# Kernel optimization log

Measured on AMD Instinct MI355X. Metric: run time of the kernel, lower is better.

Reference implementation:

```python
import jax, jax.numpy as jnp
import numpy as np

B, L, D = 4, 2048, 1024
DI = D            # d_inner = expand * d_model, expand=1
N = 8             # d_state
K = 4             # d_conv
R = 64            # dt_rank = ceil(d_model/16)
EPS = 1e-5


def setup_inputs() -> dict:
    key = jax.random.key(0)
    ks = jax.random.split(key, 10)
    hidden_states = jax.random.normal(ks[0], (B, L, D), dtype=jnp.float32)
    norm_w = jnp.ones((D,), dtype=jnp.float32)
    in_proj_w = jax.random.normal(ks[1], (2 * DI, D), dtype=jnp.float32) * 0.02
    conv_w = jax.random.normal(ks[2], (DI, 1, K), dtype=jnp.float32) * 0.2
    conv_b = jnp.zeros((DI,), dtype=jnp.float32)
    x_proj_w = jax.random.normal(ks[3], (R + 2 * N, DI), dtype=jnp.float32) * 0.02
    dt_proj_w = jax.random.normal(ks[4], (DI, R), dtype=jnp.float32) * 0.1
    # bias init so softplus(bias) lands in a sane dt range (~e^-4 .. e^-1)
    dt_proj_b = jax.random.uniform(ks[5], (DI,), minval=-4.0, maxval=-1.0, dtype=jnp.float32)
    # S4D-real style init: A = -[1..N] per channel
    A_log = jnp.log(jnp.broadcast_to(jnp.arange(1, N + 1, dtype=jnp.float32), (DI, N)))
    D_skip = jnp.ones((DI,), dtype=jnp.float32)
    out_proj_w = jax.random.normal(ks[6], (D, DI), dtype=jnp.float32) * 0.02
    return {
        "hidden_states": hidden_states, "norm_w": norm_w,
        "in_proj_w": in_proj_w, "conv_w": conv_w, "conv_b": conv_b,
        "x_proj_w": x_proj_w, "dt_proj_w": dt_proj_w, "dt_proj_b": dt_proj_b,
        "A_log": A_log, "D_skip": D_skip, "out_proj_w": out_proj_w,
    }


def _rmsnorm(x, w):
    return x * jax.lax.rsqrt(jnp.mean(x * x, axis=-1, keepdims=True) + EPS) * w


def _mamba_block(hidden_states, norm_w, in_proj_w, conv_w, conv_b,
                 x_proj_w, dt_proj_w, dt_proj_b, A_log, D_skip, out_proj_w):
    x = _rmsnorm(hidden_states, norm_w)                      # [B,L,D]
    xz = jnp.einsum('bld,ed->ble', x, in_proj_w)             # [B,L,2*DI]
    x, z = jnp.split(xz, 2, axis=-1)                         # [B,L,DI] each
    # causal depthwise conv1d (torch pads d_conv-1 both sides then slices :L => left pad only)
    xc = jnp.transpose(x, (0, 2, 1))                         # [B,DI,L]
    k = conv_w.shape[-1]
    xc = jax.lax.conv_general_dilated(
        xc, conv_w, window_strides=(1,), padding=[(k - 1, 0)],
        dimension_numbers=('NCH', 'OIH', 'NCH'), feature_group_count=DI)
    x = jax.nn.silu(jnp.transpose(xc, (0, 2, 1)) + conv_b)   # [B,L,DI]
    # input-dependent dt, B, C
    dbl = jnp.einsum('bld,ed->ble', x, x_proj_w)             # [B,L,R+2N]
    dt, Bm, Cm = jnp.split(dbl, [R, R + N], axis=-1)
    dt = jax.nn.softplus(jnp.einsum('blr,dr->bld', dt, dt_proj_w) + dt_proj_b)  # [B,L,DI]
    A = -jnp.exp(A_log)                                      # [DI,N]
    dA = jnp.exp(dt[..., None] * A)                          # [B,L,DI,N]
    dBx = dt[..., None] * Bm[:, :, None, :] * x[..., None]   # [B,L,DI,N]

    def step(h, inp):
        a_t, bx_t, c_t = inp                                 # [B,DI,N],[B,DI,N],[B,N]
        h = a_t * h + bx_t
        y = jnp.einsum('bdn,bn->bd', h, c_t)
        return h, y

    h0 = jnp.zeros((hidden_states.shape[0], DI, N), dtype=x.dtype)
    _, ys = jax.lax.scan(step, h0, (jnp.transpose(dA, (1, 0, 2, 3)),
                                    jnp.transpose(dBx, (1, 0, 2, 3)),
                                    jnp.transpose(Cm, (1, 0, 2))))
    y = jnp.transpose(ys, (1, 0, 2)) + D_skip * x            # [B,L,DI]
    y = y * jax.nn.silu(z)
    out = jnp.einsum('bld,ed->ble', y, out_proj_w)           # [B,L,D]
    return out  # use_res=False


def reference(hidden_states, norm_w, in_proj_w, conv_w, conv_b,
              x_proj_w, dt_proj_w, dt_proj_b, A_log, D_skip, out_proj_w):
    return _mamba_block(hidden_states, norm_w, in_proj_w, conv_w, conv_b,
                        x_proj_w, dt_proj_w, dt_proj_b, A_log, D_skip, out_proj_w)
```

## Files before the change

### kernel.cpp

```cpp
#include <hip/hip_runtime.h>
#include <stdint.h>
#include <stddef.h>


typedef unsigned short u16;
typedef unsigned int u32;
typedef _Float16 f16;
typedef __attribute__((ext_vector_type(8))) _Float16 half8;
typedef __attribute__((ext_vector_type(4))) _Float16 half4;
typedef __attribute__((ext_vector_type(4))) float f32x4;

#define LSEQ 2048
#define DMODEL 1024
#define NSTATE 8
#define NCHUNK 64
#define CHUNKL 32
#define NROWS 8192
#define WS_NEED (115ull << 20)

__device__ __forceinline__ void gload_lds16(const void* g, void* l) {
    __builtin_amdgcn_global_load_lds((__attribute__((address_space(1))) void*)g,
                                     (__attribute__((address_space(3))) void*)l,
                                     16, 0, 0);
}

__global__ __launch_bounds__(256) void sentinel_kernel(float* __restrict__ out, int n) {
    int i = blockIdx.x * 256 + threadIdx.x;
    if (i < n) out[i] = 999.0f;
}

#define T0 524288
#define T1 20480
#define T2 16384
#define T3 262144
#define WCVT_BLK 3216
#define ZERO_BLK 640
__global__ __launch_bounds__(256) void prep_kernel(const float* __restrict__ s0,
                                                   const float* __restrict__ s1,
                                                   const float* __restrict__ s2,
                                                   const float* __restrict__ s3,
                                                   f16* __restrict__ d0, f16* __restrict__ d1,
                                                   f16* __restrict__ d2, f16* __restrict__ d3,
                                                   float* __restrict__ dblz,
                                                   const float* __restrict__ X,
                                                   const float* __restrict__ W,
                                                   f16* __restrict__ O) {
    const int bx = blockIdx.x;
    const int tid = threadIdx.x;
    if (bx < WCVT_BLK) {
        int idx = bx * 256 + tid;
        const float* s; f16* d; int i;
        if (idx < T0) { s = s0; d = d0; i = idx; }
        else if (idx < T0 + T1) { s = s1; d = d1; i = idx - T0; }
        else if (idx < T0 + T1 + T2) { s = s2; d = d2; i = idx - T0 - T1; }
        else { s = s3; d = d3; i = idx - T0 - T1 - T2; }
        f32x4 v = *(const f32x4*)(s + (size_t)i * 4);
        half4 o; o[0] = (f16)v[0]; o[1] = (f16)v[1]; o[2] = (f16)v[2]; o[3] = (f16)v[3];
        *(half4*)(d + (size_t)i * 4) = o;
    } else if (bx < WCVT_BLK + ZERO_BLK) {
        int i = (bx - WCVT_BLK) * 256 + tid;
        const f32x4 z4 = {0.f, 0.f, 0.f, 0.f};
        ((f32x4*)dblz)[i] = z4;
    } else {
        const int row = bx - (WCVT_BLK + ZERO_BLK);
        f32x4 u = *(const f32x4*)(X + (size_t)row * DMODEL + tid * 4);
        float ss = u[0]*u[0] + u[1]*u[1] + u[2]*u[2] + u[3]*u[3];
        for (int off = 32; off; off >>= 1) ss += __shfl_down(ss, off, 64);
        __shared__ float red[4];
        if ((tid & 63) == 0) red[tid >> 6] = ss;
        __syncthreads();
        float tot = red[0] + red[1] + red[2] + red[3];
        float scale = rsqrtf(tot * (1.0f / DMODEL) + 1e-5f);
        f32x4 w = *(const f32x4*)(W + tid * 4);
        half4 o;
        o[0] = (f16)(u[0] * scale * w[0]); o[1] = (f16)(u[1] * scale * w[1]);
        o[2] = (f16)(u[2] * scale * w[2]); o[3] = (f16)(u[3] * scale * w[3]);
        *(half4*)(O + (size_t)row * DMODEL + tid * 4) = o;
    }
}

template <int EPI, int AF32>
__global__ __launch_bounds__(256) void gemm_f16(const void* __restrict__ Ap, int lda,
                                                const f16* __restrict__ Bm, int ldb,
                                                void* __restrict__ C0, void* __restrict__ C1,
                                                int ldc, int N, int klen,
                                                const float* __restrict__ fbias) {
    __shared__ alignas(16) f16 sA[128 * 64];
    __shared__ alignas(16) f16 sB[128 * 64];
    const int tid = threadIdx.x;
    const int wave = tid >> 6, lane = tid & 63;
    const int wm = (wave >> 1) * 64, wn = (wave & 1) * 64;
    const int tm = blockIdx.x, tn = blockIdx.y;
    const int q = lane >> 4, cl = lane & 15;
    const int kbeg = blockIdx.z * klen;

    f32x4 acc[4][4];
    const f32x4 zero4 = {0.f, 0.f, 0.f, 0.f};
#pragma unroll
    for (int t = 0; t < 4; t++)
#pragma unroll
        for (int u = 0; u < 4; u++) acc[t][u] = zero4;

    int rS[4], gkS[4];
#pragma unroll
    for (int j = 0; j < 4; j++) {
        int c = wave * 256 + j * 64 + lane;
        rS[j] = c >> 3;
        gkS[j] = (c & 7) ^ (rS[j] & 7);
    }

    for (int k0 = kbeg; k0 < kbeg + klen; k0 += 64) {
        __syncthreads();
#pragma unroll
        for (int j = 0; j < 4; j++) {
            int ldsoff = (wave * 256 + j * 64) * 8;
            if (!AF32) {
                int ga = tm * 128 + rS[j];
                gload_lds16((const f16*)Ap + (size_t)ga * lda + k0 + gkS[j] * 8, sA + ldsoff);
            }
            int gb = tn * 128 + rS[j];
            if (gb >= N) gb = N - 1;
            gload_lds16(Bm + (size_t)gb * ldb + k0 + gkS[j] * 8, sB + ldsoff);
        }
        __syncthreads();

        half8 af[4][2], bf[4][2];
#pragma unroll
        for (int t = 0; t < 4; t++)
#pragma unroll
            for (int s = 0; s < 2; s++) {
                int m = wm + t * 16 + cl;
                int kc = s * 4 + q;
                if (AF32) {
                    const float* pa = (const float*)Ap + (size_t)(tm * 128 + m) * lda + k0 + kc * 8;
                    f32x4 v0 = *(const f32x4*)pa, v1 = *(const f32x4*)(pa + 4);
                    half8 a;
                    a[0] = (f16)v0[0]; a[1] = (f16)v0[1]; a[2] = (f16)v0[2]; a[3] = (f16)v0[3];
                    a[4] = (f16)v1[0]; a[5] = (f16)v1[1]; a[6] = (f16)v1[2]; a[7] = (f16)v1[3];
                    af[t][s] = a;
                } else {
                    af[t][s] = *(const half8*)(sA + m * 64 + ((kc ^ (m & 7)) << 3));
                }
                int n = wn + t * 16 + cl;
                bf[t][s] = *(const half8*)(sB + n * 64 + ((kc ^ (n & 7)) << 3));
            }
#pragma unroll
        for (int t = 0; t < 4; t++)
#pragma unroll
            for (int u = 0; u < 4; u++) {
                acc[t][u] = __builtin_amdgcn_mfma_f32_16x16x32_f16(af[t][0], bf[u][0], acc[t][u], 0, 0, 0);
                acc[t][u] = __builtin_amdgcn_mfma_f32_16x16x32_f16(af[t][1], bf[u][1], acc[t][u], 0, 0, 0);
            }
    }

    const int rowbase = tm * 128 + wm + q * 4;
    const int colbase = tn * 128 + wn + cl;
#pragma unroll
    for (int t = 0; t < 4; t++)
#pragma unroll
        for (int r = 0; r < 4; r++) {
            size_t rb_ = (size_t)(rowbase + t * 16 + r) * ldc;
            size_t rb1 = (size_t)(rowbase + t * 16 + r) * 1024;
#pragma unroll
            for (int u = 0; u < 4; u++) {
                int gcol = colbase + u * 16;
                float v = acc[t][u][r];
                if (EPI == 0) {
                    if (gcol < 1024) ((f16*)C0)[rb1 + gcol] = (f16)v;
                    else             ((f16*)C1)[rb1 + gcol - 1024] = (f16)v;
                } else if (EPI == 1) {
                    if (gcol < N) ((float*)C0)[rb_ + gcol] = v;
                } else if (EPI == 2) {
                    if (gcol < N) atomicAdd((float*)C0 + rb_ + gcol, v);
                } else {
                    if (gcol < N) {
                        float sv = v + fbias[gcol];
                        sv = (sv > 15.f) ? sv : log1pf(__expf(sv));
                        ((f16*)C0)[rb_ + gcol] = (f16)sv;
                    }
                }
            }
        }
}

__global__ __launch_bounds__(256) void conv_silu_kernel(const f16* __restrict__ x,
                                                        const float* __restrict__ cw,
                                                        const float* __restrict__ cb,
                                                        f16* __restrict__ xc) {
    const int rg = blockIdx.x;
    const int d = blockIdx.y * 256 + threadIdx.x;
    const int row0 = rg * 4;
    const int l0 = row0 & (LSEQ - 1);
    float w0 = cw[d * 4], w1 = cw[d * 4 + 1], w2 = cw[d * 4 + 2], w3 = cw[d * 4 + 3];
    float bias = cb[d];
    float v[7];
#pragma unroll
    for (int j = 0; j < 7; j++) {
        int ll = l0 - 3 + j;
        v[j] = (ll >= 0) ? (float)x[(size_t)(row0 - 3 + j) * 1024 + d] : 0.f;
    }
#pragma unroll
    for (int i = 0; i < 4; i++) {
        float acc = bias + w0 * v[i] + w1 * v[i + 1] + w2 * v[i + 2] + w3 * v[i + 3];
        xc[(size_t)(row0 + i) * 1024 + d] = (f16)(acc / (1.f + __expf(-acc)));
    }
}

__global__ __launch_bounds__(256) void scan1_kernel(const f16* __restrict__ dt,
                                                    const f16* __restrict__ xc,
                                                    const float* __restrict__ dbl,
                                                    const float* __restrict__ A_log,
                                                    float* __restrict__ hF,
                                                    float* __restrict__ Pb) {
    const int d = blockIdx.x * 256 + threadIdx.x;
    const int c = blockIdx.y;
    const int b = blockIdx.z;
    __shared__ float sB[CHUNKL * NSTATE];
    sB[threadIdx.x] = dbl[(size_t)(b * LSEQ + c * CHUNKL + (threadIdx.x >> 3)) * 80 + 64 + (threadIdx.x & 7)];
    __syncthreads();
    f32x4 al0 = *(const f32x4*)(A_log + d * 8);
    f32x4 al1 = *(const f32x4*)(A_log + d * 8 + 4);
    float Aa[NSTATE];
#pragma unroll
    for (int n = 0; n < 4; n++) { Aa[n] = -__expf(al0[n]); Aa[n + 4] = -__expf(al1[n]); }
    float h[NSTATE], P[NSTATE];
#pragma unroll
    for (int n = 0; n < NSTATE; n++) { h[n] = 0.f; P[n] = 1.f; }
    const f16* pdt = dt + (size_t)(b * LSEQ + c * CHUNKL) * 1024 + d;
    const f16* pxc = xc + (size_t)(b * LSEQ + c * CHUNKL) * 1024 + d;
    for (int lb = 0; lb < CHUNKL; lb += 8) {
        float vdt[8], vxc[8];
#pragma unroll
        for (int j = 0; j < 8; j++) {
            vdt[j] = (float)pdt[(size_t)(lb + j) * 1024];
            vxc[j] = (float)pxc[(size_t)(lb + j) * 1024];
        }
#pragma unroll
        for (int j = 0; j < 8; j++) {
            float dtx = vdt[j] * vxc[j];
#pragma unroll
            for (int n = 0; n < NSTATE; n++) {
                float e = __expf(Aa[n] * vdt[j]);
                h[n] = e * h[n] + dtx * sB[(lb + j) * 8 + n];
                P[n] *= e;
            }
        }
    }
    size_t base = ((size_t)(c * 4 + b) * 1024 + d) * 8;
    f32x4 o;
    o[0]=h[0]; o[1]=h[1]; o[2]=h[2]; o[3]=h[3]; *(f32x4*)(hF + base) = o;
    o[0]=h[4]; o[1]=h[5]; o[2]=h[6]; o[3]=h[7]; *(f32x4*)(hF + base + 4) = o;
    o[0]=P[0]; o[1]=P[1]; o[2]=P[2]; o[3]=P[3]; *(f32x4*)(Pb + base) = o;
    o[0]=P[4]; o[1]=P[5]; o[2]=P[6]; o[3]=P[7]; *(f32x4*)(Pb + base + 4) = o;
}

__global__ __launch_bounds__(256) void combine_kernel(const float* __restrict__ hF,
                                                      const float* __restrict__ Pb,
                                                      float* __restrict__ h0) {
    int t = blockIdx.x * 256 + threadIdx.x;
    int n = t & 7, dd = (t >> 3) & 1023, b = t >> 13;
    size_t off = (size_t)(b * 1024 + dd) * 8 + n;
    float h = 0.f;
#pragma unroll 8
    for (int c = 0; c < NCHUNK; c++) {
        size_t idx = (size_t)c * 32768 + off;
        h0[idx] = h;
        h = fmaf(Pb[idx], h, hF[idx]);
    }
}

__global__ __launch_bounds__(256) void scan2_kernel(const f16* __restrict__ dt,
                                                    const f16* __restrict__ xc,
                                                    const float* __restrict__ dbl,
                                                    const float* __restrict__ A_log,
                                                    const float* __restrict__ h0,
                                                    const f16* __restrict__ z,
                                                    const float* __restrict__ Dsk,
                                                    f16* __restrict__ yout) {
    const int d = blockIdx.x * 256 + threadIdx.x;
    const int c = blockIdx.y;
    const int b = blockIdx.z;
    __shared__ float sB[CHUNKL * NSTATE];
    __shared__ float sC[CHUNKL * NSTATE];
    {
        size_t rb = (size_t)(b * LSEQ + c * CHUNKL + (threadIdx.x >> 3)) * 80;
        sB[threadIdx.x] = dbl[rb + 64 + (threadIdx.x & 7)];
        sC[threadIdx.x] = dbl[rb + 72 + (threadIdx.x & 7)];
    }
    __syncthreads();
    f32x4 al0 = *(const f32x4*)(A_log + d * 8);
    f32x4 al1 = *(const f32x4*)(A_log + d * 8 + 4);
    float Aa[NSTATE];
#pragma unroll
    for (int n = 0; n < 4; n++) { Aa[n] = -__expf(al0[n]); Aa[n + 4] = -__expf(al1[n]); }
    float h[NSTATE];
    {
        size_t base = ((size_t)(c * 4 + b) * 1024 + d) * 8;
        f32x4 h0a = *(const f32x4*)(h0 + base);
        f32x4 h0b = *(const f32x4*)(h0 + base + 4);
#pragma unroll
        for (int n = 0; n < 4; n++) { h[n] = h0a[n]; h[n + 4] = h0b[n]; }
    }
    const float dval = Dsk[d];
    const size_t rowoff = (size_t)(b * LSEQ + c * CHUNKL) * 1024 + d;
    const f16* pdt = dt + rowoff;
    const f16* pxc = xc + rowoff;
    const f16* pz  = z  + rowoff;
    f16* py = yout + rowoff;
    for (int lb = 0; lb < CHUNKL; lb += 8) {
        float vdt[8], vxc[8], vz[8];
#pragma unroll
        for (int j = 0; j < 8; j++) {
            vdt[j] = (float)pdt[(size_t)(lb + j) * 1024];
            vxc[j] = (float)pxc[(size_t)(lb + j) * 1024];
            vz[j]  = (float)pz[(size_t)(lb + j) * 1024];
        }
#pragma unroll
        for (int j = 0; j < 8; j++) {
            float dtx = vdt[j] * vxc[j];
            float y = 0.f;
#pragma unroll
            for (int n = 0; n < NSTATE; n++) {
                float e = __expf(Aa[n] * vdt[j]);
                h[n] = e * h[n] + dtx * sB[(lb + j) * 8 + n];
                y += h[n] * sC[(lb + j) * 8 + n];
            }
            y += dval * vxc[j];
            y *= vz[j] / (1.f + __expf(-vz[j]));
            py[(size_t)(lb + j) * 1024] = (f16)y;
        }
    }
}

extern "C" void kernel_launch(void* const* d_in, const int* in_sizes, int n_in,
                              void* d_out, int out_size, void* d_ws, size_t ws_size,
                              hipStream_t stream) {
    (void)in_sizes; (void)n_in;
    const float* hidden    = (const float*)d_in[0];
    const float* norm_w    = (const float*)d_in[1];
    const float* in_proj_w = (const float*)d_in[2];
    const float* conv_w    = (const float*)d_in[3];
    const float* conv_b    = (const float*)d_in[4];
    const float* x_proj_w  = (const float*)d_in[5];
    const float* dt_proj_w = (const float*)d_in[6];
    const float* dt_proj_b = (const float*)d_in[7];
    const float* A_log     = (const float*)d_in[8];
    const float* D_skip    = (const float*)d_in[9];
    const float* out_proj_w= (const float*)d_in[10];
    float* out = (float*)d_out;

    if (ws_size < WS_NEED) {
        sentinel_kernel<<<dim3((out_size + 255) / 256), 256, 0, stream>>>(out, out_size);
        return;
    }

    char* ws = (char*)d_ws;
    f16*   xn_h  = (f16*)(ws);
    f16*   xbuf_h= (f16*)(ws + (16ull << 20));
    f16*   zbuf_h= (f16*)(ws + (32ull << 20));
    f16*   xc_h  = (f16*)(ws + (48ull << 20));
    f16*   wih   = (f16*)(ws + (64ull << 20));
    f16*   woh   = (f16*)(ws + (68ull << 20));
    f16*   wxh   = (f16*)(ws + (70ull << 20));
    f16*   wdh   = (f16*)(ws + (70ull << 20) + (512ull << 10));
    float* dbl_f = (float*)(ws + (71ull << 20));
    f16*   dth   = (f16*)(ws + (75ull << 20));
    float* hF    = (float*)(ws + (91ull << 20));
    float* Pb    = (float*)(ws + (99ull << 20));
    float* h0    = (float*)(ws + (107ull << 20));
    f16*   y_h   = xn_h;

    prep_kernel<<<dim3(WCVT_BLK + ZERO_BLK + NROWS), 256, 0, stream>>>(
        in_proj_w, x_proj_w, dt_proj_w, out_proj_w, wih, wxh, wdh, woh,
        dbl_f, hidden, norm_w, xn_h);
    gemm_f16<0, 0><<<dim3(64, 16), 256, 0, stream>>>(xn_h, 1024, wih, 1024,
                                                     xbuf_h, zbuf_h, 1024, 2048, 1024, nullptr);
    conv_silu_kernel<<<dim3(NROWS / 4, 4), 256, 0, stream>>>(xbuf_h, conv_w, conv_b, xc_h);
    gemm_f16<2, 0><<<dim3(64, 1, 4), 256, 0, stream>>>(xc_h, 1024, wxh, 1024,
                                                       dbl_f, nullptr, 80, 80, 256, nullptr);
    gemm_f16<3, 1><<<dim3(64, 8), 256, 0, stream>>>(dbl_f, 80, wdh, 64,
                                                    dth, nullptr, 1024, 1024, 64, dt_proj_b);
    scan1_kernel<<<dim3(4, NCHUNK, 4), 256, 0, stream>>>(dth, xc_h, dbl_f, A_log, hF, Pb);
    combine_kernel<<<dim3(128), 256, 0, stream>>>(hF, Pb, h0);
    scan2_kernel<<<dim3(4, NCHUNK, 4), 256, 0, stream>>>(dth, xc_h, dbl_f, A_log, h0,
                                                         zbuf_h, D_skip, y_h);
    gemm_f16<1, 0><<<dim3(64, 8), 256, 0, stream>>>(y_h, 1024, woh, 1024,
                                                    out, nullptr, 1024, 1024, 1024, nullptr);
}
```

Baseline: 296.6 us.

## Add 256-row triple-buffered MFMA GEMM for in_proj and out_proj

Adds a new gemm256 kernel with 512 threads, 256xBN tiles, a K-step of 32, and a three-stage LDS ring filled by direct global-to-LDS loads with explicit vmcnt waits. Wave priority is raised around the MFMA loop. It replaces the 128x128 GEMM for the large in_proj (N=2048) and out_proj (N=1024) matmuls, aiming for more data reuse per tile and for global loads that overlap compute. The trade-off is fewer workgroups (256 per launch) and higher register pressure from the 8xNR accumulator tiles.

Result: slower. 433.7 us (+46.2%).

```diff
diff --git a/kernel.cpp b/kernel.cpp
--- a/kernel.cpp
+++ b/kernel.cpp
@@ -79,6 +79,121 @@
     }
 }
 
+template <int BN, int EPI>
+__global__ __launch_bounds__(512, 2) void gemm256(const f16* __restrict__ Ap, int lda,
+                                                  const f16* __restrict__ Bm, int ldb,
+                                                  void* __restrict__ C0, void* __restrict__ C1,
+                                                  int KT) {
+    constexpr int NR = BN / 64;
+    constexpr int Wn = BN / 4;
+    __shared__ alignas(16) f16 sA[3 * 256 * 32];
+    __shared__ alignas(16) f16 sB[3 * BN * 32];
+
+    const int tid = threadIdx.x;
+    const int wave = tid >> 6, lane = tid & 63;
+    const int wm = wave >> 2, wn = wave & 3;
+    const int cl = lane & 15, q = lane >> 4;
+    const int tm = blockIdx.x, tn = blockIdx.y;
+
+    const f16* aSrc[2]; int aLds[2];
+#pragma unroll
+    for (int j = 0; j < 2; j++) {
+        int c = j * 512 + tid;
+        int row = c >> 2;
+        int kc = (c & 3) ^ ((c >> 3) & 3);
+        aSrc[j] = Ap + (size_t)(tm * 256 + row) * lda + kc * 8;
+        aLds[j] = (j * 512 + wave * 64) * 8;
+    }
+    const f16* bSrc[2]; int bLds[2];
+#pragma unroll
+    for (int j = 0; j < BN / 128; j++) {
+        int c = j * 512 + tid;
+        int row = c >> 2;
+        int kc = (c & 3) ^ ((c >> 3) & 3);
+        bSrc[j] = Bm + (size_t)(tn * BN + row) * ldb + kc * 8;
+        bLds[j] = (j * 512 + wave * 64) * 8;
+    }
+
+    auto STAGE = [&](int kt, int buf) {
+        const int k0 = kt * 32;
+#pragma unroll
+        for (int j = 0; j < 2; j++)
+            gload_lds16(aSrc[j] + k0, sA + buf * (256 * 32) + aLds[j]);
+#pragma unroll
+        for (int j = 0; j < BN / 128; j++)
+            gload_lds16(bSrc[j] + k0, sB + buf * (BN * 32) + bLds[j]);
+    };
+
+    f32x4 acc[8][NR];
+    const f32x4 zero4 = {0.f, 0.f, 0.f, 0.f};
+#pragma unroll
+    for (int fr = 0; fr < 8; fr++)
+#pragma unroll
+        for (int fn = 0; fn < NR; fn++) acc[fr][fn] = zero4;
+
+    const int aswz = q ^ ((cl >> 1) & 3);
+
+    STAGE(0, 0);
+    STAGE(1, 1);
+
+    for (int t = 0; t < KT; t++) {
+        if (t < KT - 1) {
+            if constexpr (BN == 256) asm volatile("s_waitcnt vmcnt(4)" ::: "memory");
+            else                     asm volatile("s_waitcnt vmcnt(3)" ::: "memory");
+        } else {
+            asm volatile("s_waitcnt vmcnt(0)" ::: "memory");
+        }
+        __builtin_amdgcn_s_barrier();
+        asm volatile("" ::: "memory");
+        __builtin_amdgcn_sched_barrier(0);
+
+        if (t + 2 < KT) STAGE(t + 2, (t + 2) % 3);
+
+        const f16* sAb = sA + (t % 3) * (256 * 32);
+        const f16* sBb = sB + (t % 3) * (BN * 32);
+
+        half8 af[8], bf[NR];
+#pragma unroll
+        for (int fr = 0; fr < 8; fr++) {
+            int row = wm * 128 + fr * 16 + cl;
+            af[fr] = *(const half8*)(sAb + row * 32 + (aswz << 3));
+        }
+#pragma unroll
+        for (int fn = 0; fn < NR; fn++) {
+            int n = wn * Wn + fn * 16 + cl;
+            bf[fn] = *(const half8*)(sBb + n * 32 + (aswz << 3));
+        }
+
+        __builtin_amdgcn_s_setprio(1);
+#pragma unroll
+        for (int fr = 0; fr < 8; fr++)
+#pragma unroll
+            for (int fn = 0; fn < NR; fn++)
+                acc[fr][fn] = __builtin_amdgcn_mfma_f32_16x16x32_f16(af[fr], bf[fn], acc[fr][fn], 0, 0, 0);
+        __builtin_amdgcn_s_setprio(0);
+    }
+
+    const int rowb = tm * 256 + wm * 128 + q * 4;
+    const int colb = tn * BN + wn * Wn + cl;
+#pragma unroll
+    for (int fr = 0; fr < 8; fr++)
+#pragma unroll
+        for (int r = 0; r < 4; r++) {
+            size_t ro = (size_t)(rowb + fr * 16 + r) * 1024;
+#pragma unroll
+            for (int fn = 0; fn < NR; fn++) {
+                int gc = colb + fn * 16;
+                float v = acc[fr][fn][r];
+                if (EPI == 0) {
+                    if (gc < 1024) ((f16*)C0)[ro + gc] = (f16)v;
+                    else           ((f16*)C1)[ro + gc - 1024] = (f16)v;
+                } else {
+                    ((float*)C0)[ro + gc] = v;
+                }
+            }
+        }
+}
+
 template <int EPI, int AF32>
 __global__ __launch_bounds__(256) void gemm_f16(const void* __restrict__ Ap, int lda,
                                                 const f16* __restrict__ Bm, int ldb,
@@ -160,19 +275,13 @@
 #pragma unroll
         for (int r = 0; r < 4; r++) {
             size_t rb_ = (size_t)(rowbase + t * 16 + r) * ldc;
-            size_t rb1 = (size_t)(rowbase + t * 16 + r) * 1024;
 #pragma unroll
             for (int u = 0; u < 4; u++) {
                 int gcol = colbase + u * 16;
                 float v = acc[t][u][r];
-                if (EPI == 0) {
-                    if (gcol < 1024) ((f16*)C0)[rb1 + gcol] = (f16)v;
-                    else             ((f16*)C1)[rb1 + gcol - 1024] = (f16)v;
-                } else if (EPI == 1) {
-                    if (gcol < N) ((float*)C0)[rb_ + gcol] = v;
-                } else if (EPI == 2) {
+                if (EPI == 2) {
                     if (gcol < N) atomicAdd((float*)C0 + rb_ + gcol, v);
-                } else {
+                } else if (EPI == 3) {
                     if (gcol < N) {
                         float sv = v + fbias[gcol];
                         sv = (sv > 15.f) ? sv : log1pf(__expf(sv));
@@ -373,8 +482,8 @@
     prep_kernel<<<dim3(WCVT_BLK + ZERO_BLK + NROWS), 256, 0, stream>>>(
         in_proj_w, x_proj_w, dt_proj_w, out_proj_w, wih, wxh, wdh, woh,
         dbl_f, hidden, norm_w, xn_h);
-    gemm_f16<0, 0><<<dim3(64, 16), 256, 0, stream>>>(xn_h, 1024, wih, 1024,
-                                                     xbuf_h, zbuf_h, 1024, 2048, 1024, nullptr);
+    gemm256<256, 0><<<dim3(32, 8), 512, 0, stream>>>(xn_h, 1024, wih, 1024,
+                                                     xbuf_h, zbuf_h, 32);
     conv_silu_kernel<<<dim3(NROWS / 4, 4), 256, 0, stream>>>(xbuf_h, conv_w, conv_b, xc_h);
     gemm_f16<2, 0><<<dim3(64, 1, 4), 256, 0, stream>>>(xc_h, 1024, wxh, 1024,
                                                        dbl_f, nullptr, 80, 80, 256, nullptr);
@@ -384,6 +493,6 @@
     combine_kernel<<<dim3(128), 256, 0, stream>>>(hF, Pb, h0);
     scan2_kernel<<<dim3(4, NCHUNK, 4), 256, 0, stream>>>(dth, xc_h, dbl_f, A_log, h0,
                                                          zbuf_h, D_skip, y_h);
-    gemm_f16<1, 0><<<dim3(64, 8), 256, 0, stream>>>(y_h, 1024, woh, 1024,
-                                                    out, nullptr, 1024, 1024, 1024, nullptr);
-}
+    gemm256<128, 1><<<dim3(32, 8), 512, 0, stream>>>(y_h, 1024, woh, 1024,
+                                                     out, nullptr, 32);
+}
```
